# Optimization experiments

Hardware: AMD Instinct MI355X
Metric: run time of the kernel (lower is better)

The kernel has to match this reference:

```python
import jax, jax.numpy as jnp
import numpy as np

SEQ, B, IN, H = 512, 64, 256, 512

def _lin_params(key, out_d, in_d):
    k1, k2 = jax.random.split(key)
    bound = 1.0 / np.sqrt(in_d)
    w = jax.random.uniform(k1, (out_d, in_d), jnp.float32, -bound, bound)
    b = jax.random.uniform(k2, (out_d,), jnp.float32, -bound, bound)
    return w, b

def setup_inputs() -> dict:
    key = jax.random.key(0)
    ks = jax.random.split(key, 9)
    x = jax.random.normal(ks[0], (SEQ, B, IN), jnp.float32)
    h0 = jnp.zeros((B, H), jnp.float32)
    c0 = jnp.zeros((B, H), jnp.float32)
    Wf_w, Wf_b = _lin_params(ks[1], H, IN)
    Uf_w, Uf_b = _lin_params(ks[2], H, H)
    Wi_w, Wi_b = _lin_params(ks[3], H, IN)
    Ui_w, Ui_b = _lin_params(ks[4], H, H)
    Wo_w, Wo_b = _lin_params(ks[5], H, IN)
    Uo_w, Uo_b = _lin_params(ks[6], H, H)
    Wc_w, Wc_b = _lin_params(ks[7], H, IN)
    Uc_w, Uc_b = _lin_params(ks[8], H, H)
    return dict(x=x, h0=h0, c0=c0,
                Wf_w=Wf_w, Wf_b=Wf_b, Uf_w=Uf_w, Uf_b=Uf_b,
                Wi_w=Wi_w, Wi_b=Wi_b, Ui_w=Ui_w, Ui_b=Ui_b,
                Wo_w=Wo_w, Wo_b=Wo_b, Uo_w=Uo_w, Uo_b=Uo_b,
                Wc_w=Wc_w, Wc_b=Wc_b, Uc_w=Uc_w, Uc_b=Uc_b)

def reference(x, h0, c0,
              Wf_w, Wf_b, Uf_w, Uf_b,
              Wi_w, Wi_b, Ui_w, Ui_b,
              Wo_w, Wo_b, Uo_w, Uo_b,
              Wc_w, Wc_b, Uc_w, Uc_b):
    # Precompute all input-to-hidden projections in one batched GEMM per gate.
    xf = jnp.einsum('tbi,hi->tbh', x, Wf_w) + Wf_b  # (T,B,H)
    xi = jnp.einsum('tbi,hi->tbh', x, Wi_w) + Wi_b
    xo = jnp.einsum('tbi,hi->tbh', x, Wo_w) + Wo_b
    xc = jnp.einsum('tbi,hi->tbh', x, Wc_w) + Wc_b

    def step(carry, xs):
        h, c = carry
        xft, xit, xot, xct = xs
        f = jax.nn.sigmoid(xft + h @ Uf_w.T + Uf_b)
        i = jax.nn.sigmoid(xit + h @ Ui_w.T + Ui_b)
        o = jax.nn.sigmoid(xot + h @ Uo_w.T + Uo_b)
        c = f * c + i * jnp.tanh(xct + h @ Uc_w.T + Uc_b)
        h = o * jnp.tanh(c)
        return (h, c), h

    (h, c), h_seq = jax.lax.scan(step, (h0, c0), (xf, xi, xo, xc))
    return h_seq, h, c
```

## Files before the change

### kernel.cpp

```cpp
#include <hip/hip_runtime.h>


#define T_STEPS 512
#define BATCH   64
#define IN_D    256
#define HID     512
#define NGROUP  8
#define NSLICE  16
#define BLK_B   8
#define BLK_H   32
#define THREADS 512
#define NBLK    (NGROUP * NSLICE)
#define CH_ROW  128
#define SLOT_BYTES (NGROUP * BLK_B * CH_ROW * 16)
#define WARMUP   8
#define FAST_CAP 128

using short8  = __attribute__((ext_vector_type(8))) short;
using int4v   = __attribute__((ext_vector_type(4))) int;
using float4v = __attribute__((ext_vector_type(4))) float;

#define FRAG_ADDR(f) (((f) << 4) + (((f) >> 4) << 4))

__device__ __forceinline__ unsigned short f2bf(float f) {
    union { float f; unsigned int i; } v; v.f = f;
    unsigned int r = v.i + 0x7fff + ((v.i >> 16) & 1);
    return (unsigned short)(r >> 16);
}
__device__ __forceinline__ short8 pack8(float4 a, float4 b) {
    short8 s;
    s[0]=(short)f2bf(a.x); s[1]=(short)f2bf(a.y); s[2]=(short)f2bf(a.z); s[3]=(short)f2bf(a.w);
    s[4]=(short)f2bf(b.x); s[5]=(short)f2bf(b.y); s[6]=(short)f2bf(b.z); s[7]=(short)f2bf(b.w);
    return s;
}
__device__ __forceinline__ float sigm(float v) { return 1.0f / (1.0f + __expf(-v)); }
__device__ __forceinline__ float tanh_(float v) { return 2.0f / (1.0f + __expf(-2.0f * v)) - 1.0f; }

__device__ __forceinline__ void lds_barrier() {
    asm volatile("s_waitcnt lgkmcnt(0)" ::: "memory");
    __builtin_amdgcn_s_barrier();
    __builtin_amdgcn_sched_barrier(0);
}

__global__ __launch_bounds__(256, 1) void lstm_init_ws(unsigned int* w, int n) {
    int i = blockIdx.x * blockDim.x + threadIdx.x;
    if (i < n) __hip_atomic_store(&w[i], 0u, __ATOMIC_RELAXED, __HIP_MEMORY_SCOPE_AGENT);
}

__global__ __launch_bounds__(THREADS, 1) void lstm_persist(
    const float* __restrict__ x,
    const float* __restrict__ h0,
    const float* __restrict__ c0,
    const float* __restrict__ Wf, const float* __restrict__ Wfb,
    const float* __restrict__ Uf, const float* __restrict__ Ufb,
    const float* __restrict__ Wi, const float* __restrict__ Wib,
    const float* __restrict__ Ui, const float* __restrict__ Uib,
    const float* __restrict__ Wo, const float* __restrict__ Wob,
    const float* __restrict__ Uo, const float* __restrict__ Uob,
    const float* __restrict__ Wc, const float* __restrict__ Wcb,
    const float* __restrict__ Uc, const float* __restrict__ Ucb,
    float* out,
    unsigned char* ex_fast,
    unsigned char* ex_slow,
    unsigned int* ctrl)
{
    __shared__ __attribute__((aligned(16))) unsigned char hfrag[17392];
    __shared__ __attribute__((aligned(16))) unsigned char xfrag[8688];
    __shared__ float g_lds[8 * 320];
    __shared__ unsigned int warm_fail_lds;
    __shared__ unsigned int mode_lds;

    const int tid  = threadIdx.x;
    const int lane = tid & 63;
    const int wave = tid >> 6;
    const int gate = wave >> 1;
    const int hlf  = wave & 1;
    const int grp  = blockIdx.x & 7;
    const int slc  = blockIdx.x >> 3;
    const int bb   = grp * BLK_B;
    const int hbase= slc * BLK_H;
    const int lm   = lane & 15;
    const int lq   = lane >> 4;
    const int row  = tid >> 5;
    const int seg  = tid & 31;
    const int pr   = tid & 7;
    const int kb   = tid >> 3;

    const float* Ug  = (gate == 0) ? Uf : (gate == 1) ? Ui : (gate == 2) ? Uo : Uc;
    const float* Wg  = (gate == 0) ? Wf : (gate == 1) ? Wi : (gate == 2) ? Wo : Wc;
    const float* Wbg = (gate == 0) ? Wfb : (gate == 1) ? Wib : (gate == 2) ? Wob : Wcb;
    const float* Ubg = (gate == 0) ? Ufb : (gate == 1) ? Uib : (gate == 2) ? Uob : Ucb;
    const int ng = hbase + hlf * 16 + lm;

    short8 ufrag[16];
#pragma unroll
    for (int ks = 0; ks < 16; ++ks) {
        const float* p = Ug + (size_t)ng * HID + ks * 32 + lq * 8;
        ufrag[ks] = pack8(*(const float4*)(p), *(const float4*)(p + 4));
    }
    short8 wfrag[8];
#pragma unroll
    for (int ks = 0; ks < 8; ++ks) {
        const float* p = Wg + (size_t)ng * IN_D + ks * 32 + lq * 8;
        wfrag[ks] = pack8(*(const float4*)(p), *(const float4*)(p + 4));
    }
    const float bias = Wbg[ng] + Ubg[ng];

    for (int i = tid; i < 17392 / 4; i += THREADS) ((unsigned int*)hfrag)[i] = 0u;
    for (int i = tid; i < 8688 / 4;  i += THREADS) ((unsigned int*)xfrag)[i] = 0u;
    if (tid == 0) { warm_fail_lds = 0u; mode_lds = 0u; }
    __syncthreads();

    float c_reg = 0.f;
    if (row < 8) c_reg = c0[(size_t)(bb + row) * HID + hbase + seg];

    if (row < 8) {
        const float* ph = h0 + (size_t)(bb + row) * HID + seg * 16;
        int f0 = (seg >> 1) * 64 + (seg & 1) * 32 + row;
        *(short8*)(hfrag + FRAG_ADDR(f0))      = pack8(*(const float4*)(ph),     *(const float4*)(ph + 4));
        *(short8*)(hfrag + FRAG_ADDR(f0 + 16)) = pack8(*(const float4*)(ph + 8), *(const float4*)(ph + 12));
        const float* px = x + (size_t)(bb + row) * IN_D + seg * 8;
        int fx = (seg >> 2) * 64 + (seg & 3) * 16 + row;
        *(short8*)(xfrag + FRAG_ADDR(fx)) = pack8(*(const float4*)(px), *(const float4*)(px + 4));
    }
    float4 xa0 = {0,0,0,0}, xa1 = {0,0,0,0}, xb0 = {0,0,0,0}, xb1 = {0,0,0,0};
    if (row < 8) {
        const float* px = x + ((size_t)1 * BATCH + bb + row) * IN_D + seg * 8;
        xa0 = *(const float4*)(px); xa1 = *(const float4*)(px + 4);
    }
    __syncthreads();

    float4v accx0 = {bias, bias, bias, bias};
    float4v accx1 = {0.f, 0.f, 0.f, 0.f};
#pragma unroll
    for (int ks = 0; ks < 8; ++ks) {
        short8 a = *(const short8*)(xfrag + FRAG_ADDR(ks * 64 + lane));
        if (ks & 1) accx1 = __builtin_amdgcn_mfma_f32_16x16x32_bf16(a, wfrag[ks], accx1, 0, 0, 0);
        else        accx0 = __builtin_amdgcn_mfma_f32_16x16x32_bf16(a, wfrag[ks], accx0, 0, 0, 0);
    }

    float* const out_h = out + (size_t)T_STEPS * BATCH * HID;
    float* const out_c = out_h + (size_t)BATCH * HID;

    unsigned char* const fa_wr = ex_fast + (size_t)((bb + row) * CH_ROW + slc * 8 + (seg >> 2)) * 16;
    unsigned char* const sl_wr = ex_slow + (size_t)((bb + row) * CH_ROW + slc * 8 + (seg >> 2)) * 16;
    const unsigned char* const fa_rd = ex_fast + (size_t)((bb + pr) * CH_ROW + kb * 2) * 16;
    const unsigned char* const sl_rd = ex_slow + (size_t)((bb + pr) * CH_ROW + kb * 2) * 16;

    int mode = 0;

    auto STEP = [&](int t, float4& sx0, float4& sx1, float4& px0, float4& px1) {
        if (t == WARMUP) {
            if (tid == 0) {
                if (warm_fail_lds)
                    __hip_atomic_store(&ctrl[0], 1u, __ATOMIC_RELAXED, __HIP_MEMORY_SCOPE_AGENT);
                asm volatile("s_waitcnt vmcnt(0)" ::: "memory");
                __hip_atomic_fetch_add(&ctrl[1], 1u, __ATOMIC_RELAXED, __HIP_MEMORY_SCOPE_AGENT);
                long g = 0;
                while (__hip_atomic_load(&ctrl[1], __ATOMIC_RELAXED, __HIP_MEMORY_SCOPE_AGENT) < (unsigned)NBLK
                       && ++g < (1L << 26)) { }
                mode_lds = __hip_atomic_load(&ctrl[0], __ATOMIC_RELAXED, __HIP_MEMORY_SCOPE_AGENT);
            }
            __syncthreads();
            mode = (int)mode_lds;
        }
        const bool warm = (t < WARMUP);

        if (row < 8) {
            int tn = (t + 2 < T_STEPS) ? (t + 2) : (T_STEPS - 1);
            const float* px = x + ((size_t)tn * BATCH + bb + row) * IN_D + seg * 8;
            px0 = *(const float4*)(px); px1 = *(const float4*)(px + 4);
        }

        float4v acc0 = accx0, acc1 = accx1;
#pragma unroll
        for (int ks = 0; ks < 16; ++ks) {
            short8 a = *(const short8*)(hfrag + FRAG_ADDR(ks * 64 + lane));
            if (ks & 1) acc1 = __builtin_amdgcn_mfma_f32_16x16x32_bf16(a, ufrag[ks], acc1, 0, 0, 0);
            else        acc0 = __builtin_amdgcn_mfma_f32_16x16x32_bf16(a, ufrag[ks], acc0, 0, 0, 0);
        }
        float4v acc = acc0 + acc1;
#pragma unroll
        for (int r = 0; r < 4; ++r)
            g_lds[wave * 320 + lq * 80 + r * 16 + lm] = acc[r];

        if (t + 1 < T_STEPS && row < 8) {
            int fx = (seg >> 2) * 64 + (seg & 3) * 16 + row;
            *(short8*)(xfrag + FRAG_ADDR(fx)) = pack8(sx0, sx1);
        }

        lds_barrier();

        float hv = 0.f;
        if (row < 8) {
            int hf2 = seg >> 4, nn = seg & 15;
            int rbase = (row >> 2) * 80 + (row & 3) * 16 + nn;
            float fpre = g_lds[(0 * 2 + hf2) * 320 + rbase];
            float ipre = g_lds[(1 * 2 + hf2) * 320 + rbase];
            float opre = g_lds[(2 * 2 + hf2) * 320 + rbase];
            float gpre = g_lds[(3 * 2 + hf2) * 320 + rbase];
            float fv = sigm(fpre), iv = sigm(ipre), ov = sigm(opre);
            float gv = tanh_(gpre);
            c_reg = fv * c_reg + iv * gv;
            hv = ov * tanh_(c_reg);
            out[((size_t)t * BATCH + bb + row) * HID + hbase + seg] = hv;
        }

        if (t + 1 < T_STEPS) {
            if (row < 8) {
                unsigned int bfv = f2bf(hv);
                unsigned int nb  = (unsigned int)__shfl_xor((int)bfv, 1);
                unsigned int p   = bfv | (nb << 16);
                unsigned int q   = (unsigned int)__shfl_xor((int)p, 2);
                if ((tid & 3) == 0) {
                    int4v ch; ch[0] = (int)p; ch[1] = (int)q; ch[2] = t + 1; ch[3] = 0;
                    const size_t so = (size_t)(t & 1) * SLOT_BYTES;
                    if (warm || mode == 0)
                        asm volatile("global_store_dwordx4 %0, %1, off sc0"
                                     :: "v"(fa_wr + so), "v"(ch) : "memory");
                    if (warm || mode == 1)
                        asm volatile("global_store_dwordx4 %0, %1, off sc0 sc1"
                                     :: "v"(sl_wr + so), "v"(ch) : "memory");
                }
            }

            accx0 = (float4v){bias, bias, bias, bias};
            accx1 = (float4v){0.f, 0.f, 0.f, 0.f};
#pragma unroll
            for (int ks = 0; ks < 8; ++ks) {
                short8 a = *(const short8*)(xfrag + FRAG_ADDR(ks * 64 + lane));
                if (ks & 1) accx1 = __builtin_amdgcn_mfma_f32_16x16x32_bf16(a, wfrag[ks], accx1, 0, 0, 0);
                else        accx0 = __builtin_amdgcn_mfma_f32_16x16x32_bf16(a, wfrag[ks], accx0, 0, 0, 0);
            }

            const int want = t + 1;
            const size_t so = (size_t)(t & 1) * SLOT_BYTES;
            int4v e0, e1;
            bool got = false;
            if (warm || mode == 0) {
                const unsigned char* pb = fa_rd + so;
                long cap = warm ? (long)FAST_CAP : (1L << 24);
                for (long it = 0; it < cap; ++it) {
                    asm volatile(
                        "global_load_dwordx4 %0, %2, off sc0\n\t"
                        "global_load_dwordx4 %1, %2, off offset:16 sc0\n\t"
                        "s_waitcnt vmcnt(0)"
                        : "=&v"(e0), "=&v"(e1) : "v"(pb) : "memory");
                    if ((e0[2] == want) & (e1[2] == want)) { got = true; break; }
                }
            }
            if (!got) {
                if (warm) warm_fail_lds = 1u;
                const unsigned char* pb = sl_rd + so;
                long guard = 0;
                for (;;) {
                    asm volatile(
                        "global_load_dwordx4 %0, %2, off sc0 sc1\n\t"
                        "global_load_dwordx4 %1, %2, off offset:16 sc0 sc1\n\t"
                        "s_waitcnt vmcnt(0)"
                        : "=&v"(e0), "=&v"(e1) : "v"(pb) : "memory");
                    if ((e0[2] == want) & (e1[2] == want)) break;
                    if (++guard > (1L << 24)) break;
                }
            }
            int f0 = (kb >> 2) * 64 + (kb & 3) * 16 + pr;
            *(int4v*)(hfrag + FRAG_ADDR(f0)) = (int4v){e0[0], e0[1], e1[0], e1[1]};

            lds_barrier();
        } else {
            if (row < 8) {
                out_h[(size_t)(bb + row) * HID + hbase + seg] = hv;
                out_c[(size_t)(bb + row) * HID + hbase + seg] = c_reg;
            }
        }
    };

    for (int t = 0; t < T_STEPS; t += 2) {
        STEP(t,     xa0, xa1, xb0, xb1);
        STEP(t + 1, xb0, xb1, xa0, xa1);
    }
}

extern "C" void kernel_launch(void* const* d_in, const int* in_sizes, int n_in,
                              void* d_out, int out_size, void* d_ws, size_t ws_size,
                              hipStream_t stream) {
    (void)in_sizes; (void)n_in; (void)out_size;
    const float* x   = (const float*)d_in[0];
    const float* h0  = (const float*)d_in[1];
    const float* c0  = (const float*)d_in[2];
    const float* Wf  = (const float*)d_in[3];
    const float* Wfb = (const float*)d_in[4];
    const float* Uf  = (const float*)d_in[5];
    const float* Ufb = (const float*)d_in[6];
    const float* Wi  = (const float*)d_in[7];
    const float* Wib = (const float*)d_in[8];
    const float* Ui  = (const float*)d_in[9];
    const float* Uib = (const float*)d_in[10];
    const float* Wo  = (const float*)d_in[11];
    const float* Wob = (const float*)d_in[12];
    const float* Uo  = (const float*)d_in[13];
    const float* Uob = (const float*)d_in[14];
    const float* Wc  = (const float*)d_in[15];
    const float* Wcb = (const float*)d_in[16];
    const float* Uc  = (const float*)d_in[17];
    const float* Ucb = (const float*)d_in[18];

    unsigned char* base = (unsigned char*)d_ws;
    unsigned char* ex_fast = base;
    unsigned char* ex_slow;
    size_t used;
    if (ws_size >= 4 * (size_t)SLOT_BYTES + 64) {
        ex_slow = base + 2 * (size_t)SLOT_BYTES;
        used = 4 * (size_t)SLOT_BYTES + 64;
    } else {
        ex_slow = base;
        used = 2 * (size_t)SLOT_BYTES + 64;
    }
    unsigned int* ctrl = (unsigned int*)(base + used - 64);

    const int nzero = (int)(used / 4);
    lstm_init_ws<<<(nzero + 255) / 256, 256, 0, stream>>>((unsigned int*)base, nzero);
    lstm_persist<<<NBLK, THREADS, 0, stream>>>(
        x, h0, c0,
        Wf, Wfb, Uf, Ufb, Wi, Wib, Ui, Uib,
        Wo, Wob, Uo, Uob, Wc, Wcb, Uc, Ucb,
        (float*)d_out, ex_fast, ex_slow, ctrl);
}
```

Baseline: 1.827 ms.

## Assign batch groups by XCC so exchange stays within one die's L2

At startup each block reads its hardware XCC id and claims a slice index inside a group tied to that XCC. All blocks sharing a batch group therefore run on the same die and can exchange h over the fast non-coherent path through a shared L2. If any XCC receives more than NSLICE blocks, the kernel falls back to the slow coherent exchange. It also moves the per-step h output store and the x prefetch to after the exchange wait, so they no longer delay the critical-path publish. It adds a startup grid barrier and relies on the hardware placement of blocks across XCCs.

```diff
diff --git a/kernel.cpp b/kernel.cpp
--- a/kernel.cpp
+++ b/kernel.cpp
@@ -12,9 +12,8 @@
 #define THREADS 512
 #define NBLK    (NGROUP * NSLICE)
 #define CH_ROW  128
-#define SLOT_BYTES (NGROUP * BLK_B * CH_ROW * 16)
-#define WARMUP   8
-#define FAST_CAP 128
+#define SLOT_BYTES (BATCH * CH_ROW * 16)
+#define WARMUP  8
 
 using short8  = __attribute__((ext_vector_type(8))) short;
 using int4v   = __attribute__((ext_vector_type(4))) int;
@@ -67,18 +66,13 @@
     __shared__ __attribute__((aligned(16))) unsigned char hfrag[17392];
     __shared__ __attribute__((aligned(16))) unsigned char xfrag[8688];
     __shared__ float g_lds[8 * 320];
-    __shared__ unsigned int warm_fail_lds;
-    __shared__ unsigned int mode_lds;
+    __shared__ unsigned int s_ok, s_grp, s_slc, s_mode, warm_fail;
 
     const int tid  = threadIdx.x;
     const int lane = tid & 63;
     const int wave = tid >> 6;
     const int gate = wave >> 1;
     const int hlf  = wave & 1;
-    const int grp  = blockIdx.x & 7;
-    const int slc  = blockIdx.x >> 3;
-    const int bb   = grp * BLK_B;
-    const int hbase= slc * BLK_H;
     const int lm   = lane & 15;
     const int lq   = lane >> 4;
     const int row  = tid >> 5;
@@ -86,6 +80,29 @@
     const int pr   = tid & 7;
     const int kb   = tid >> 3;
 
+    if (tid == 0) {
+        unsigned int xcc = (unsigned int)__builtin_amdgcn_s_getreg((31u << 11) | 20u) & 7u;
+        unsigned int sc  = __hip_atomic_fetch_add(&ctrl[xcc], 1u,
+                               __ATOMIC_RELAXED, __HIP_MEMORY_SCOPE_AGENT);
+        if (sc >= (unsigned)NSLICE)
+            __hip_atomic_store(&ctrl[9], 1u, __ATOMIC_RELAXED, __HIP_MEMORY_SCOPE_AGENT);
+        asm volatile("s_waitcnt vmcnt(0)" ::: "memory");
+        __hip_atomic_fetch_add(&ctrl[8], 1u, __ATOMIC_RELAXED, __HIP_MEMORY_SCOPE_AGENT);
+        long g = 0;
+        while (__hip_atomic_load(&ctrl[8], __ATOMIC_RELAXED, __HIP_MEMORY_SCOPE_AGENT)
+                   < (unsigned)NBLK && ++g < (1L << 24)) { }
+        unsigned int bad = __hip_atomic_load(&ctrl[9], __ATOMIC_RELAXED, __HIP_MEMORY_SCOPE_AGENT);
+        if (g >= (1L << 24)) bad = 1u;
+        s_ok = bad ? 0u : 1u; s_grp = xcc; s_slc = sc;
+        warm_fail = 0u;
+    }
+    __syncthreads();
+    const int claim_ok = (int)s_ok;
+    const int grp  = claim_ok ? (int)s_grp : (blockIdx.x & 7);
+    const int slc  = claim_ok ? (int)s_slc : (int)(blockIdx.x >> 3);
+    const int bb   = grp * BLK_B;
+    const int hbase= slc * BLK_H;
+
     const float* Ug  = (gate == 0) ? Uf : (gate == 1) ? Ui : (gate == 2) ? Uo : Uc;
     const float* Wg  = (gate == 0) ? Wf : (gate == 1) ? Wi : (gate == 2) ? Wo : Wc;
     const float* Wbg = (gate == 0) ? Wfb : (gate == 1) ? Wib : (gate == 2) ? Wob : Wcb;
@@ -108,7 +125,6 @@
 
     for (int i = tid; i < 17392 / 4; i += THREADS) ((unsigned int*)hfrag)[i] = 0u;
     for (int i = tid; i < 8688 / 4;  i += THREADS) ((unsigned int*)xfrag)[i] = 0u;
-    if (tid == 0) { warm_fail_lds = 0u; mode_lds = 0u; }
     __syncthreads();
 
     float c_reg = 0.f;
@@ -142,35 +158,29 @@
     float* const out_h = out + (size_t)T_STEPS * BATCH * HID;
     float* const out_c = out_h + (size_t)BATCH * HID;
 
-    unsigned char* const fa_wr = ex_fast + (size_t)((bb + row) * CH_ROW + slc * 8 + (seg >> 2)) * 16;
-    unsigned char* const sl_wr = ex_slow + (size_t)((bb + row) * CH_ROW + slc * 8 + (seg >> 2)) * 16;
-    const unsigned char* const fa_rd = ex_fast + (size_t)((bb + pr) * CH_ROW + kb * 2) * 16;
-    const unsigned char* const sl_rd = ex_slow + (size_t)((bb + pr) * CH_ROW + kb * 2) * 16;
-
-    int mode = 0;
+    const size_t wr_off = (size_t)((bb + row) * CH_ROW + slc * 8 + (seg >> 2)) * 16;
+    const size_t rd_off = (size_t)((bb + pr) * CH_ROW + kb * 2) * 16;
+
+    int mode = claim_ok ? 0 : 1;
 
     auto STEP = [&](int t, float4& sx0, float4& sx1, float4& px0, float4& px1) {
         if (t == WARMUP) {
             if (tid == 0) {
-                if (warm_fail_lds)
-                    __hip_atomic_store(&ctrl[0], 1u, __ATOMIC_RELAXED, __HIP_MEMORY_SCOPE_AGENT);
+                if (warm_fail)
+                    __hip_atomic_store(&ctrl[11], 1u, __ATOMIC_RELAXED, __HIP_MEMORY_SCOPE_AGENT);
                 asm volatile("s_waitcnt vmcnt(0)" ::: "memory");
-                __hip_atomic_fetch_add(&ctrl[1], 1u, __ATOMIC_RELAXED, __HIP_MEMORY_SCOPE_AGENT);
+                __hip_atomic_fetch_add(&ctrl[10], 1u, __ATOMIC_RELAXED, __HIP_MEMORY_SCOPE_AGENT);
                 long g = 0;
-                while (__hip_atomic_load(&ctrl[1], __ATOMIC_RELAXED, __HIP_MEMORY_SCOPE_AGENT) < (unsigned)NBLK
-                       && ++g < (1L << 26)) { }
-                mode_lds = __hip_atomic_load(&ctrl[0], __ATOMIC_RELAXED, __HIP_MEMORY_SCOPE_AGENT);
+                while (__hip_atomic_load(&ctrl[10], __ATOMIC_RELAXED, __HIP_MEMORY_SCOPE_AGENT)
+                           < (unsigned)NBLK && ++g < (1L << 24)) { }
+                unsigned int b = __hip_atomic_load(&ctrl[11], __ATOMIC_RELAXED, __HIP_MEMORY_SCOPE_AGENT);
+                if (g >= (1L << 24)) b = 1u;
+                s_mode = (claim_ok && !b) ? 0u : 1u;
             }
             __syncthreads();
-            mode = (int)mode_lds;
+            mode = (int)s_mode;
         }
         const bool warm = (t < WARMUP);
-
-        if (row < 8) {
-            int tn = (t + 2 < T_STEPS) ? (t + 2) : (T_STEPS - 1);
-            const float* px = x + ((size_t)tn * BATCH + bb + row) * IN_D + seg * 8;
-            px0 = *(const float4*)(px); px1 = *(const float4*)(px + 4);
-        }
 
         float4v acc0 = accx0, acc1 = accx1;
 #pragma unroll
@@ -203,24 +213,26 @@
             float gv = tanh_(gpre);
             c_reg = fv * c_reg + iv * gv;
             hv = ov * tanh_(c_reg);
-            out[((size_t)t * BATCH + bb + row) * HID + hbase + seg] = hv;
         }
 
         if (t + 1 < T_STEPS) {
+            const size_t so = (size_t)(t & 1) * SLOT_BYTES;
+            const unsigned int want = (unsigned int)(t + 1);
+
             if (row < 8) {
                 unsigned int bfv = f2bf(hv);
                 unsigned int nb  = (unsigned int)__shfl_xor((int)bfv, 1);
                 unsigned int p   = bfv | (nb << 16);
                 unsigned int q   = (unsigned int)__shfl_xor((int)p, 2);
                 if ((tid & 3) == 0) {
-                    int4v ch; ch[0] = (int)p; ch[1] = (int)q; ch[2] = t + 1; ch[3] = 0;
-                    const size_t so = (size_t)(t & 1) * SLOT_BYTES;
-                    if (warm || mode == 0)
+                    int4v ch; ch[0] = (int)p; ch[1] = (int)q;
+                    ch[2] = (int)want; ch[3] = (int)want;
+                    if ((warm && claim_ok) || (!warm && mode == 0))
                         asm volatile("global_store_dwordx4 %0, %1, off sc0"
-                                     :: "v"(fa_wr + so), "v"(ch) : "memory");
+                                     :: "v"(ex_fast + wr_off + so), "v"(ch) : "memory");
                     if (warm || mode == 1)
                         asm volatile("global_store_dwordx4 %0, %1, off sc0 sc1"
-                                     :: "v"(sl_wr + so), "v"(ch) : "memory");
+                                     :: "v"(ex_slow + wr_off + so), "v"(ch) : "memory");
                 }
             }
 
@@ -233,25 +245,24 @@
                 else        accx0 = __builtin_amdgcn_mfma_f32_16x16x32_bf16(a, wfrag[ks], accx0, 0, 0, 0);
             }
 
-            const int want = t + 1;
-            const size_t so = (size_t)(t & 1) * SLOT_BYTES;
             int4v e0, e1;
             bool got = false;
-            if (warm || mode == 0) {
-                const unsigned char* pb = fa_rd + so;
-                long cap = warm ? (long)FAST_CAP : (1L << 24);
+            if ((warm && claim_ok) || (!warm && mode == 0)) {
+                const unsigned char* pb = ex_fast + rd_off + so;
+                long cap = warm ? 64L : (1L << 22);
                 for (long it = 0; it < cap; ++it) {
                     asm volatile(
                         "global_load_dwordx4 %0, %2, off sc0\n\t"
                         "global_load_dwordx4 %1, %2, off offset:16 sc0\n\t"
                         "s_waitcnt vmcnt(0)"
                         : "=&v"(e0), "=&v"(e1) : "v"(pb) : "memory");
-                    if ((e0[2] == want) & (e1[2] == want)) { got = true; break; }
+                    if (((unsigned int)e0[2] == want) & ((unsigned int)e0[3] == want) &
+                        ((unsigned int)e1[2] == want) & ((unsigned int)e1[3] == want)) { got = true; break; }
                 }
             }
-            if (!got) {
-                if (warm) warm_fail_lds = 1u;
-                const unsigned char* pb = sl_rd + so;
+            if (!got && (warm || mode == 1)) {
+                if (warm) warm_fail = 1u;
+                const unsigned char* pb = ex_slow + rd_off + so;
                 long guard = 0;
                 for (;;) {
                     asm volatile(
@@ -259,16 +270,26 @@
                         "global_load_dwordx4 %1, %2, off offset:16 sc0 sc1\n\t"
                         "s_waitcnt vmcnt(0)"
                         : "=&v"(e0), "=&v"(e1) : "v"(pb) : "memory");
-                    if ((e0[2] == want) & (e1[2] == want)) break;
-                    if (++guard > (1L << 24)) break;
+                    if (((unsigned int)e0[2] == want) & ((unsigned int)e1[2] == want)) break;
+                    if (++guard > (1L << 22)) break;
                 }
             }
             int f0 = (kb >> 2) * 64 + (kb & 3) * 16 + pr;
             *(int4v*)(hfrag + FRAG_ADDR(f0)) = (int4v){e0[0], e0[1], e1[0], e1[1]};
+
+            if (row < 8)
+                out[((size_t)t * BATCH + bb + row) * HID + hbase + seg] = hv;
+
+            if (row < 8) {
+                int tn = (t + 2 < T_STEPS) ? (t + 2) : (T_STEPS - 1);
+                const float* px = x + ((size_t)tn * BATCH + bb + row) * IN_D + seg * 8;
+                px0 = *(const float4*)(px); px1 = *(const float4*)(px + 4);
+            }
 
             lds_barrier();
         } else {
             if (row < 8) {
+                out[((size_t)t * BATCH + bb + row) * HID + hbase + seg] = hv;
                 out_h[(size_t)(bb + row) * HID + hbase + seg] = hv;
                 out_c[(size_t)(bb + row) * HID + hbase + seg] = c_reg;
             }
```

Result: faster. 1.730 ms (-5.3%).
